# Optimization experiments

Measured on AMD Instinct MI355X. Metric: run time of the kernel, lower is better.

The kernel has to match this reference:

```python
import jax, jax.numpy as jnp
import numpy as np

EMBED_DIM = 1024
NUM_HEADS = 16
HEAD_DIM = EMBED_DIM // NUM_HEADS


def setup_inputs() -> dict:
    key = jax.random.key(0)
    ks = jax.random.split(key, 9)
    B, S, E = 2, 2048, EMBED_DIM
    lim = 1.0 / np.sqrt(E)
    def lin(kw, kb):
        W = jax.random.uniform(kw, (E, E), jnp.float32, -lim, lim)
        b = jax.random.uniform(kb, (E,), jnp.float32, -lim, lim)
        return W, b
    Wq, bq = lin(ks[0], ks[1])
    Wk, bk = lin(ks[2], ks[3])
    Wv, bv = lin(ks[4], ks[5])
    Wo, bo = lin(ks[6], ks[7])
    x = jax.random.normal(ks[8], (B, S, E), jnp.float32)
    return {"x": x, "Wq": Wq, "bq": bq, "Wk": Wk, "bk": bk,
            "Wv": Wv, "bv": bv, "Wo": Wo, "bo": bo}


def reference(x, Wq, bq, Wk, bk, Wv, bv, Wo, bo):
    B, S, E = x.shape
    H, D = NUM_HEADS, HEAD_DIM
    scale = D ** -0.5
    # projections (torch Linear: x @ W.T + b); here W stored as [in, out]-equivalent via transpose convention
    q = (x @ Wq.T + bq).reshape(B, S, H, D).transpose(0, 2, 1, 3)  # b h s d
    k = (x @ Wk.T + bk).reshape(B, S, H, D).transpose(0, 2, 1, 3)
    v = (x @ Wv.T + bv).reshape(B, S, H, D).transpose(0, 2, 1, 3)
    scores = jnp.einsum('bhqd,bhkd->bhqk', q, k) * scale
    attn = jax.nn.softmax(scores, axis=-1)
    out = jnp.einsum('bhqk,bhkd->bhqd', attn, v)
    out = out.transpose(0, 2, 1, 3).reshape(B, S, E)
    return out @ Wo.T + bo
```

## Files before the change

kernel.cpp:

```cpp
#include <hip/hip_runtime.h>


using u16 = unsigned short;
using u32 = unsigned int;

typedef __bf16 bf16x8 __attribute__((ext_vector_type(8)));
typedef float  f32x4  __attribute__((ext_vector_type(4)));
typedef float  f32x16 __attribute__((ext_vector_type(16)));
typedef u32    u32x4  __attribute__((ext_vector_type(4)));

constexpr int GB = 2;
constexpr int GS = 2048;
constexpr int GH = 16;
constexpr int GD = 64;
constexpr int GE = 1024;
constexpr int GM = GB * GS;
constexpr int PSTRIDE = 2048;

__device__ __forceinline__ u16 f2bf(float f) {
    u32 u = __float_as_uint(f);
    u += 0x7FFFu + ((u >> 16) & 1u);
    return (u16)(u >> 16);
}

__device__ __forceinline__ void plswap(u32& a, u32& b) {
#if __has_builtin(__builtin_amdgcn_permlane32_swap)
    auto r = __builtin_amdgcn_permlane32_swap(a, b, false, false);
    a = r[0]; b = r[1];
#else
    asm volatile("v_permlane32_swap_b32 %0, %1" : "+v"(a), "+v"(b));
#endif
}

__device__ __forceinline__ float xchg32(float v) {
    u32 a = __float_as_uint(v), b = a;
    plswap(a, b);
    return __uint_as_float((threadIdx.x & 32) ? a : b);
}

__device__ __forceinline__ u32 cvtpk(float lo, float hi) {
    u32 d;
    asm("v_cvt_pk_bf16_f32 %0, %1, %2" : "=v"(d) : "v"(lo), "v"(hi));
    return d;
}

__device__ __forceinline__ void gl_lds16(const u16* g, u16* l) {
#if __has_builtin(__builtin_amdgcn_global_load_lds)
    __builtin_amdgcn_global_load_lds(
        (const __attribute__((address_space(1))) void*)g,
        (__attribute__((address_space(3))) void*)l, 16, 0, 0);
#else
    *reinterpret_cast<uint4*>(l) = *reinterpret_cast<const uint4*>(g);
#endif
}

__global__ void cvt_kernel(const float* __restrict__ in, u16* __restrict__ out, int n) {
    int idx = blockIdx.x * blockDim.x + threadIdx.x;
    int stride = gridDim.x * blockDim.x;
    for (int i = idx * 4; i < n; i += stride * 4) {
        float4 f = *reinterpret_cast<const float4*>(in + i);
        ushort4 o;
        o.x = f2bf(f.x); o.y = f2bf(f.y); o.z = f2bf(f.z); o.w = f2bf(f.w);
        *reinterpret_cast<ushort4*>(out + i) = o;
    }
}

__global__ void cvtw_kernel(const float* __restrict__ w0, const float* __restrict__ w1,
                            const float* __restrict__ w2, const float* __restrict__ w3,
                            u16* __restrict__ o0, u16* __restrict__ o1,
                            u16* __restrict__ o2, u16* __restrict__ o3) {
    const float* in = blockIdx.y == 0 ? w0 : blockIdx.y == 1 ? w1 : blockIdx.y == 2 ? w2 : w3;
    u16* out = blockIdx.y == 0 ? o0 : blockIdx.y == 1 ? o1 : blockIdx.y == 2 ? o2 : o3;
    int idx = blockIdx.x * blockDim.x + threadIdx.x;
    int stride = gridDim.x * blockDim.x;
    for (int i = idx * 4; i < GE * GE; i += stride * 4) {
        float4 f = *reinterpret_cast<const float4*>(in + i);
        ushort4 o;
        o.x = f2bf(f.x); o.y = f2bf(f.y); o.z = f2bf(f.z); o.w = f2bf(f.w);
        *reinterpret_cast<ushort4*>(out + i) = o;
    }
}

__global__ __launch_bounds__(256)
void qkv_gemm(const u16* __restrict__ A,
              const u16* __restrict__ wq, const u16* __restrict__ wk, const u16* __restrict__ wv,
              const float* __restrict__ bq, const float* __restrict__ bk, const float* __restrict__ bv,
              u16* __restrict__ Qb, u16* __restrict__ Kb, u16* __restrict__ VTb) {
    constexpr int Kd = GE;
    __shared__ u16 As[128 * 32];
    __shared__ u16 Bs[128 * 32];

    const int z = blockIdx.z;
    const u16* __restrict__ Bw = z == 0 ? wq : z == 1 ? wk : wv;
    const float* __restrict__ bias = z == 0 ? bq : z == 1 ? bk : bv;
    u16* __restrict__ outp = z == 0 ? Qb : z == 1 ? Kb : VTb;

    const int tid = threadIdx.x;
    const int m0 = blockIdx.y * 128;
    const int n0 = blockIdx.x * 128;
    const int wave = tid >> 6, lane = tid & 63;
    const int wm = (wave >> 1) * 64, wn = (wave & 1) * 64;
    const int g = lane >> 4, rw = lane & 15;

    f32x4 acc[4][4] = {};

    for (int kt = 0; kt < Kd; kt += 32) {
        __syncthreads();
#pragma unroll
        for (int j = 0; j < 2; ++j) {
            int c = wave * 128 + j * 64 + lane;
            int r = c >> 2, u = (c & 3) * 8;
            gl_lds16(&A [(size_t)(m0 + r) * Kd + kt + u], &As[c * 8]);
            gl_lds16(&Bw[(size_t)(n0 + r) * Kd + kt + u], &Bs[c * 8]);
        }
        __syncthreads();

        bf16x8 aF[4], bF[4];
#pragma unroll
        for (int mf = 0; mf < 4; ++mf)
            aF[mf] = *reinterpret_cast<const bf16x8*>(&As[(wm + mf * 16 + rw) * 32 + g * 8]);
#pragma unroll
        for (int nf = 0; nf < 4; ++nf)
            bF[nf] = *reinterpret_cast<const bf16x8*>(&Bs[(wn + nf * 16 + rw) * 32 + g * 8]);
#pragma unroll
        for (int mf = 0; mf < 4; ++mf)
#pragma unroll
            for (int nf = 0; nf < 4; ++nf)
                acc[mf][nf] = __builtin_amdgcn_mfma_f32_16x16x32_bf16(aF[mf], bF[nf], acc[mf][nf], 0, 0, 0);
    }

#pragma unroll
    for (int mf = 0; mf < 4; ++mf)
#pragma unroll
        for (int nf = 0; nf < 4; ++nf)
#pragma unroll
            for (int r = 0; r < 4; ++r) {
                int m = m0 + wm + mf * 16 + g * 4 + r;
                int n = n0 + wn + nf * 16 + rw;
                u16 hv = f2bf(acc[mf][nf][r] + bias[n]);
                int b = m >> 11, s = m & (GS - 1);
                int h = n >> 6, d = n & 63;
                if (z == 2)
                    outp[(((size_t)(b * GH + h)) * GD + d) * GS + s] = hv;
                else
                    outp[(((size_t)(b * GH + h)) * GS + s) * GD + d] = hv;
            }
}

__global__ __launch_bounds__(256)
void out_gemm(const u16* __restrict__ A, const u16* __restrict__ Bw,
              const float* __restrict__ bias, float* __restrict__ outp) {
    constexpr int Kd = GE, Nd = GE;
    __shared__ u16 As[128 * 32];
    __shared__ u16 Bs[128 * 32];

    const int tid = threadIdx.x;
    const int m0 = blockIdx.y * 128;
    const int n0 = blockIdx.x * 128;
    const int wave = tid >> 6, lane = tid & 63;
    const int wm = (wave >> 1) * 64, wn = (wave & 1) * 64;
    const int g = lane >> 4, rw = lane & 15;

    f32x4 acc[4][4] = {};

    for (int kt = 0; kt < Kd; kt += 32) {
        __syncthreads();
#pragma unroll
        for (int j = 0; j < 2; ++j) {
            int c = wave * 128 + j * 64 + lane;
            int r = c >> 2, u = (c & 3) * 8;
            gl_lds16(&A [(size_t)(m0 + r) * Kd + kt + u], &As[c * 8]);
            gl_lds16(&Bw[(size_t)(n0 + r) * Kd + kt + u], &Bs[c * 8]);
        }
        __syncthreads();

        bf16x8 aF[4], bF[4];
#pragma unroll
        for (int mf = 0; mf < 4; ++mf)
            aF[mf] = *reinterpret_cast<const bf16x8*>(&As[(wm + mf * 16 + rw) * 32 + g * 8]);
#pragma unroll
        for (int nf = 0; nf < 4; ++nf)
            bF[nf] = *reinterpret_cast<const bf16x8*>(&Bs[(wn + nf * 16 + rw) * 32 + g * 8]);
#pragma unroll
        for (int mf = 0; mf < 4; ++mf)
#pragma unroll
            for (int nf = 0; nf < 4; ++nf)
                acc[mf][nf] = __builtin_amdgcn_mfma_f32_16x16x32_bf16(aF[mf], bF[nf], acc[mf][nf], 0, 0, 0);
    }

#pragma unroll
    for (int mf = 0; mf < 4; ++mf)
#pragma unroll
        for (int nf = 0; nf < 4; ++nf)
#pragma unroll
            for (int r = 0; r < 4; ++r) {
                int m = m0 + wm + mf * 16 + g * 4 + r;
                int n = n0 + wn + nf * 16 + rw;
                outp[(size_t)m * Nd + n] = acc[mf][nf][r] + bias[n];
            }
}

template <int NSPLIT>
__global__ __launch_bounds__(256)
void attn_kernel(const u16* __restrict__ Q, const u16* __restrict__ Kp,
                 const u16* __restrict__ VT, u16* __restrict__ ctx,
                 float* __restrict__ Opart, float* __restrict__ Mpart,
                 float* __restrict__ Lpart) {
    int bh, qb, split;
    if (NSPLIT == 2) {
        const int wg = (blockIdx.x & 7) * 128 + (blockIdx.x >> 3);
        bh = wg >> 5;
        split = wg & 1;
        qb = ((wg >> 1) & 15) * 128;
    } else {
        const int wg = (blockIdx.x & 7) * 64 + (blockIdx.x >> 3);
        bh = wg >> 4;
        split = 0;
        qb = (wg & 15) * 128;
    }
    const int wave = threadIdx.x >> 6;
    const int lane = threadIdx.x & 63;
    const int l31 = lane & 31;
    const int hi = lane >> 5;
    const int q0 = qb + wave * 32;
    constexpr int KVLEN = GS / NSPLIT;
    constexpr int NT2 = KVLEN / 64;
    const int kvbase = split * KVLEN;

    const u16* __restrict__ Qbh = Q  + (size_t)bh * GS * GD;
    const u16* __restrict__ Kbh = Kp + (size_t)bh * GS * GD;
    const u16* __restrict__ Vbh = VT + (size_t)bh * GD * GS;

    __shared__ u16 sK[2][4096];
    __shared__ u16 sV[2][4096];

    bf16x8 qf[4];
#pragma unroll
    for (int s = 0; s < 4; ++s)
        qf[s] = *reinterpret_cast<const bf16x8*>(
            Qbh + (size_t)(q0 + l31) * GD + hi * 8 + 16 * s);

    f32x16 O0 = {}, O1 = {};
    float m = -1e30f, lsum = 0.f;
    const float SC = 0.125f * 1.44269504088896f;

    const int c0 = wave * 128 + lane;
    const int r0 = c0 >> 3, w0 = c0 & 7;
    const int swzcol = (w0 ^ (r0 & 7)) * 8;
    const u16* kSrc = Kbh + (size_t)(kvbase + r0) * GD + swzcol;
    const u16* vSrc = Vbh + (size_t)r0 * GS + kvbase + swzcol;
    u16* const dK0 = &sK[0][c0 * 8];
    u16* const dK1 = &sK[1][c0 * 8];
    u16* const dV0 = &sV[0][c0 * 8];
    u16* const dV1 = &sV[1][c0 * 8];

    auto stageTo = [&](u16* dk, u16* dv, const u16* ks, const u16* vs) {
        gl_lds16(ks,            dk);
        gl_lds16(ks + 8 * GD,   dk + 512);
        gl_lds16(vs,            dv);
        gl_lds16(vs + 8 * GS,   dv + 512);
    };

    int offA[4];
#pragma unroll
    for (int s = 0; s < 4; ++s)
        offA[s] = l31 * 64 + (((2 * s + hi) ^ (l31 & 7)) * 8);

    auto step = [&](const u16* bK, const u16* bV) {
        f32x16 sa = {}, sb = {};
        bf16x8 ka[4], kb[4];
#pragma unroll
        for (int s = 0; s < 4; ++s) {
            ka[s] = *reinterpret_cast<const bf16x8*>(&bK[offA[s]]);
            kb[s] = *reinterpret_cast<const bf16x8*>(&bK[offA[s] + 2048]);
        }
        __builtin_amdgcn_s_setprio(1);
#pragma unroll
        for (int s = 0; s < 4; ++s) {
            sa = __builtin_amdgcn_mfma_f32_32x32x16_bf16(ka[s], qf[s], sa, 0, 0, 0);
            sb = __builtin_amdgcn_mfma_f32_32x32x16_bf16(kb[s], qf[s], sb, 0, 0, 0);
        }
        __builtin_amdgcn_s_setprio(0);

        bf16x8 vf0[4], vf1[4];
#pragma unroll
        for (int s = 0; s < 4; ++s) {
            vf0[s] = *reinterpret_cast<const bf16x8*>(&bV[offA[s]]);
            vf1[s] = *reinterpret_cast<const bf16x8*>(&bV[offA[s] + 2048]);
        }

        float t16[16];
#pragma unroll
        for (int r = 0; r < 16; ++r) t16[r] = fmaxf(sa[r], sb[r]);
        float u0 = fmaxf(fmaxf(t16[0],  t16[1]),  t16[2]);
        float u1 = fmaxf(fmaxf(t16[3],  t16[4]),  t16[5]);
        float u2 = fmaxf(fmaxf(t16[6],  t16[7]),  t16[8]);
        float u3 = fmaxf(fmaxf(t16[9],  t16[10]), t16[11]);
        float u4 = fmaxf(fmaxf(t16[12], t16[13]), t16[14]);
        float w0_ = fmaxf(fmaxf(u0, u1), u2);
        float w1_ = fmaxf(fmaxf(u3, u4), t16[15]);
        float mx = fmaxf(w0_, w1_);
        mx = fmaxf(mx, xchg32(mx));
        float mxs = mx * SC;
        if (__any(mxs > m + 8.f)) {
            float mn = fmaxf(m, mxs);
            float alpha = __builtin_amdgcn_exp2f(m - mn);
            m = mn;
            lsum *= alpha;
#pragma unroll
            for (int r = 0; r < 16; ++r) { O0[r] *= alpha; O1[r] *= alpha; }
        }
        float pa[16], pb[16];
#pragma unroll
        for (int r = 0; r < 16; ++r) {
            pa[r] = __builtin_amdgcn_exp2f(fmaf(sa[r], SC, -m));
            pb[r] = __builtin_amdgcn_exp2f(fmaf(sb[r], SC, -m));
        }
        float s16[16];
#pragma unroll
        for (int r = 0; r < 16; ++r) s16[r] = pa[r] + pb[r];
#pragma unroll
        for (int r = 0; r < 8; ++r) s16[r] += s16[r + 8];
#pragma unroll
        for (int r = 0; r < 4; ++r) s16[r] += s16[r + 4];
        lsum += (s16[0] + s16[1]) + (s16[2] + s16[3]);

        u32 wa[8], wb[8];
#pragma unroll
        for (int i = 0; i < 8; ++i) {
            wa[i] = cvtpk(pa[2 * i], pa[2 * i + 1]);
            wb[i] = cvtpk(pb[2 * i], pb[2 * i + 1]);
        }
        plswap(wa[0], wa[2]); plswap(wa[1], wa[3]);
        plswap(wa[4], wa[6]); plswap(wa[5], wa[7]);
        plswap(wb[0], wb[2]); plswap(wb[1], wb[3]);
        plswap(wb[4], wb[6]); plswap(wb[5], wb[7]);
        u32x4 a0 = {wa[0], wa[1], wa[2], wa[3]};
        u32x4 a1 = {wa[4], wa[5], wa[6], wa[7]};
        u32x4 b0 = {wb[0], wb[1], wb[2], wb[3]};
        u32x4 b1 = {wb[4], wb[5], wb[6], wb[7]};
        bf16x8 pva0 = __builtin_bit_cast(bf16x8, a0);
        bf16x8 pva1 = __builtin_bit_cast(bf16x8, a1);
        bf16x8 pvb0 = __builtin_bit_cast(bf16x8, b0);
        bf16x8 pvb1 = __builtin_bit_cast(bf16x8, b1);

        __builtin_amdgcn_s_setprio(1);
        O0 = __builtin_amdgcn_mfma_f32_32x32x16_bf16(vf0[0], pva0, O0, 0, 0, 0);
        O0 = __builtin_amdgcn_mfma_f32_32x32x16_bf16(vf0[1], pva1, O0, 0, 0, 0);
        O0 = __builtin_amdgcn_mfma_f32_32x32x16_bf16(vf0[2], pvb0, O0, 0, 0, 0);
        O0 = __builtin_amdgcn_mfma_f32_32x32x16_bf16(vf0[3], pvb1, O0, 0, 0, 0);
        O1 = __builtin_amdgcn_mfma_f32_32x32x16_bf16(vf1[0], pva0, O1, 0, 0, 0);
        O1 = __builtin_amdgcn_mfma_f32_32x32x16_bf16(vf1[1], pva1, O1, 0, 0, 0);
        O1 = __builtin_amdgcn_mfma_f32_32x32x16_bf16(vf1[2], pvb0, O1, 0, 0, 0);
        O1 = __builtin_amdgcn_mfma_f32_32x32x16_bf16(vf1[3], pvb1, O1, 0, 0, 0);
        __builtin_amdgcn_s_setprio(0);
        __syncthreads();
    };

    stageTo(dK0, dV0, kSrc, vSrc);
    kSrc += 64 * GD; vSrc += 64;
    __syncthreads();

#pragma unroll 1
    for (int t = 0; t < NT2; t += 2) {
        stageTo(dK1, dV1, kSrc, vSrc);
        kSrc += 64 * GD; vSrc += 64;
        step(sK[0], sV[0]);
        if (t + 2 < NT2) {
            stageTo(dK0, dV0, kSrc, vSrc);
            kSrc += 64 * GD; vSrc += 64;
        }
        step(sK[1], sV[1]);
    }

    lsum += xchg32(lsum);

    if (NSPLIT == 2) {
        const int wt = bh * 64 + (q0 >> 5);
        const size_t base = ((size_t)wt * 2 + split) * PSTRIDE;
#pragma unroll
        for (int r = 0; r < 16; ++r) {
            int d = (r & 3) + 8 * (r >> 2) + 4 * hi;
            Opart[base + (size_t)d * 32 + l31]        = O0[r];
            Opart[base + (size_t)(d + 32) * 32 + l31] = O1[r];
        }
        if (hi == 0) {
            Mpart[(wt * 2 + split) * 32 + l31] = m;
            Lpart[(wt * 2 + split) * 32 + l31] = lsum;
        }
    } else {
        const int bb = bh >> 4, h = bh & 15;
        const float inv = 1.0f / lsum;
        u16* crow = ctx + ((size_t)(bb * GS + q0 + l31)) * GE + h * 64;
#pragma unroll
        for (int g2 = 0; g2 < 4; ++g2) {
            ushort4 st0, st1;
            st0.x = f2bf(O0[4 * g2 + 0] * inv); st0.y = f2bf(O0[4 * g2 + 1] * inv);
            st0.z = f2bf(O0[4 * g2 + 2] * inv); st0.w = f2bf(O0[4 * g2 + 3] * inv);
            st1.x = f2bf(O1[4 * g2 + 0] * inv); st1.y = f2bf(O1[4 * g2 + 1] * inv);
            st1.z = f2bf(O1[4 * g2 + 2] * inv); st1.w = f2bf(O1[4 * g2 + 3] * inv);
            *reinterpret_cast<ushort4*>(crow + 8 * g2 + 4 * hi)      = st0;
            *reinterpret_cast<ushort4*>(crow + 32 + 8 * g2 + 4 * hi) = st1;
        }
    }
}

__global__ __launch_bounds__(256)
void combine_kernel(const float* __restrict__ Opart, const float* __restrict__ Mpart,
                    const float* __restrict__ Lpart, u16* __restrict__ ctx) {
    const int wt = blockIdx.x;
    const int bh = wt >> 6, bb = bh >> 4, h = bh & 15;
    const int q0 = (wt & 63) * 32;
    const int q = threadIdx.x & 31, db = threadIdx.x >> 5;
    const size_t b0 = (size_t)wt * 2 * PSTRIDE, b1 = b0 + PSTRIDE;

    float m0 = Mpart[(wt * 2 + 0) * 32 + q], m1 = Mpart[(wt * 2 + 1) * 32 + q];
    float l0 = Lpart[(wt * 2 + 0) * 32 + q], l1 = Lpart[(wt * 2 + 1) * 32 + q];
    float M = fmaxf(m0, m1);
    float c0 = exp2f(m0 - M), c1 = exp2f(m1 - M);
    float inv = 1.f / (c0 * l0 + c1 * l1);
    c0 *= inv; c1 *= inv;

    u16* crow = ctx + ((size_t)(bb * GS + q0 + q)) * GE + h * 64 + db * 8;
    ushort4 s0, s1;
    float o[8];
#pragma unroll
    for (int i = 0; i < 8; ++i) {
        int d = db * 8 + i;
        o[i] = c0 * Opart[b0 + (size_t)d * 32 + q] + c1 * Opart[b1 + (size_t)d * 32 + q];
    }
    s0.x = f2bf(o[0]); s0.y = f2bf(o[1]); s0.z = f2bf(o[2]); s0.w = f2bf(o[3]);
    s1.x = f2bf(o[4]); s1.y = f2bf(o[5]); s1.z = f2bf(o[6]); s1.w = f2bf(o[7]);
    *reinterpret_cast<ushort4*>(crow)     = s0;
    *reinterpret_cast<ushort4*>(crow + 4) = s1;
}

extern "C" void kernel_launch(void* const* d_in, const int* in_sizes, int n_in,
                              void* d_out, int out_size, void* d_ws, size_t ws_size,
                              hipStream_t stream) {
    (void)in_sizes; (void)n_in; (void)out_size;

    const float* x  = (const float*)d_in[0];
    const float* Wq = (const float*)d_in[1];
    const float* bq = (const float*)d_in[2];
    const float* Wk = (const float*)d_in[3];
    const float* bk = (const float*)d_in[4];
    const float* Wv = (const float*)d_in[5];
    const float* bv = (const float*)d_in[6];
    const float* Wo = (const float*)d_in[7];
    const float* bo = (const float*)d_in[8];
    float* out = (float*)d_out;

    char* ws = (char*)d_ws;
    u16* xb  = (u16*)(ws);
    u16* wqb = (u16*)(ws + (8ll  << 20));
    u16* wkb = (u16*)(ws + (10ll << 20));
    u16* wvb = (u16*)(ws + (12ll << 20));
    u16* wob = (u16*)(ws + (14ll << 20));
    u16* Qb  = (u16*)(ws + (16ll << 20));
    u16* Kb  = (u16*)(ws + (24ll << 20));
    u16* VTb = (u16*)(ws + (32ll << 20));
    u16* ctx = (u16*)(ws + (40ll << 20));
    float* Opart = (float*)(ws + (48ll << 20));
    float* Mpart = (float*)(ws + (80ll << 20));
    float* Lpart = (float*)(ws + (80ll << 20) + (512ll << 10));
    const bool split2 = ws_size >= (81ll << 20);

    cvt_kernel<<<2048, 256, 0, stream>>>(x, xb, GM * GE);
    cvtw_kernel<<<dim3(512, 4), 256, 0, stream>>>(Wq, Wk, Wv, Wo, wqb, wkb, wvb, wob);

    qkv_gemm<<<dim3(GE / 128, GM / 128, 3), 256, 0, stream>>>(
        xb, wqb, wkb, wvb, bq, bk, bv, Qb, Kb, VTb);

    if (split2) {
        attn_kernel<2><<<dim3(1024), 256, 0, stream>>>(Qb, Kb, VTb, ctx, Opart, Mpart, Lpart);
        combine_kernel<<<dim3(2048), 256, 0, stream>>>(Opart, Mpart, Lpart, ctx);
    } else {
        attn_kernel<1><<<dim3(512), 256, 0, stream>>>(Qb, Kb, VTb, ctx, Opart, Mpart, Lpart);
    }

    out_gemm<<<dim3(GE / 128, GM / 128), 256, 0, stream>>>(ctx, wob, bo, out);
}
```

Baseline: 136.0 us.

## Triple-buffer attention K/V staging and software-pipeline QK with softmax/PV

The attention loop moves from a double-buffered LDS ring to a triple-buffered one and splits each step into issueQK, readV and finish phases. The QK MFMAs for the next tile now issue before the softmax and PV work of the current tile, so matrix and vector work can overlap across tiles. Separately, the x and weight fp32-to-bf16 conversion kernels are merged into one launch. The change uses 50% more LDS per block, which may lower occupancy, and holds two sets of score and V fragments in registers at once.

New measurement: 175.6 us. 29.1% more time.

```diff
diff --git a/kernel.cpp b/kernel.cpp
--- a/kernel.cpp
+++ b/kernel.cpp
@@ -54,26 +54,19 @@
 #endif
 }
 
-__global__ void cvt_kernel(const float* __restrict__ in, u16* __restrict__ out, int n) {
+__global__ void cvt_all(const float* __restrict__ x,
+                        const float* __restrict__ w1, const float* __restrict__ w2,
+                        const float* __restrict__ w3, const float* __restrict__ w4,
+                        u16* __restrict__ ox,
+                        u16* __restrict__ o1, u16* __restrict__ o2,
+                        u16* __restrict__ o3, u16* __restrict__ o4) {
+    const int y = blockIdx.y;
+    const float* in = y == 0 ? x : y == 1 ? w1 : y == 2 ? w2 : y == 3 ? w3 : w4;
+    u16* out = y == 0 ? ox : y == 1 ? o1 : y == 2 ? o2 : y == 3 ? o3 : o4;
+    const int n = y == 0 ? GM * GE : GE * GE;
     int idx = blockIdx.x * blockDim.x + threadIdx.x;
     int stride = gridDim.x * blockDim.x;
     for (int i = idx * 4; i < n; i += stride * 4) {
-        float4 f = *reinterpret_cast<const float4*>(in + i);
-        ushort4 o;
-        o.x = f2bf(f.x); o.y = f2bf(f.y); o.z = f2bf(f.z); o.w = f2bf(f.w);
-        *reinterpret_cast<ushort4*>(out + i) = o;
-    }
-}
-
-__global__ void cvtw_kernel(const float* __restrict__ w0, const float* __restrict__ w1,
-                            const float* __restrict__ w2, const float* __restrict__ w3,
-                            u16* __restrict__ o0, u16* __restrict__ o1,
-                            u16* __restrict__ o2, u16* __restrict__ o3) {
-    const float* in = blockIdx.y == 0 ? w0 : blockIdx.y == 1 ? w1 : blockIdx.y == 2 ? w2 : w3;
-    u16* out = blockIdx.y == 0 ? o0 : blockIdx.y == 1 ? o1 : blockIdx.y == 2 ? o2 : o3;
-    int idx = blockIdx.x * blockDim.x + threadIdx.x;
-    int stride = gridDim.x * blockDim.x;
-    for (int i = idx * 4; i < GE * GE; i += stride * 4) {
         float4 f = *reinterpret_cast<const float4*>(in + i);
         ushort4 o;
         o.x = f2bf(f.x); o.y = f2bf(f.y); o.z = f2bf(f.z); o.w = f2bf(f.w);
@@ -231,8 +224,8 @@
     const u16* __restrict__ Kbh = Kp + (size_t)bh * GS * GD;
     const u16* __restrict__ Vbh = VT + (size_t)bh * GD * GS;
 
-    __shared__ u16 sK[2][4096];
-    __shared__ u16 sV[2][4096];
+    __shared__ u16 sK[3][4096];
+    __shared__ u16 sV[3][4096];
 
     bf16x8 qf[4];
 #pragma unroll
@@ -245,20 +238,17 @@
     const float SC = 0.125f * 1.44269504088896f;
 
     const int c0 = wave * 128 + lane;
-    const int r0 = c0 >> 3, w0 = c0 & 7;
-    const int swzcol = (w0 ^ (r0 & 7)) * 8;
-    const u16* kSrc = Kbh + (size_t)(kvbase + r0) * GD + swzcol;
-    const u16* vSrc = Vbh + (size_t)r0 * GS + kvbase + swzcol;
-    u16* const dK0 = &sK[0][c0 * 8];
-    u16* const dK1 = &sK[1][c0 * 8];
-    u16* const dV0 = &sV[0][c0 * 8];
-    u16* const dV1 = &sV[1][c0 * 8];
-
-    auto stageTo = [&](u16* dk, u16* dv, const u16* ks, const u16* vs) {
-        gl_lds16(ks,            dk);
-        gl_lds16(ks + 8 * GD,   dk + 512);
-        gl_lds16(vs,            dv);
-        gl_lds16(vs + 8 * GS,   dv + 512);
+    const int r0 = c0 >> 3, w0c = c0 & 7;
+    const int swzcol = (w0c ^ (r0 & 7)) * 8;
+    const u16* kStage = Kbh + (size_t)(kvbase + r0) * GD + swzcol;
+    const u16* vStage = Vbh + (size_t)r0 * GS + kvbase + swzcol;
+
+    auto stageTo = [&](int b) {
+        gl_lds16(kStage,          &sK[b][c0 * 8]);
+        gl_lds16(kStage + 8 * GD, &sK[b][c0 * 8 + 512]);
+        gl_lds16(vStage,          &sV[b][c0 * 8]);
+        gl_lds16(vStage + 8 * GS, &sV[b][c0 * 8 + 512]);
+        kStage += 64 * GD; vStage += 64;
     };
 
     int offA[4];
@@ -266,14 +256,14 @@
     for (int s = 0; s < 4; ++s)
         offA[s] = l31 * 64 + (((2 * s + hi) ^ (l31 & 7)) * 8);
 
-    auto step = [&](const u16* bK, const u16* bV) {
-        f32x16 sa = {}, sb = {};
+    auto issueQK = [&](int b, f32x16& sa, f32x16& sb) {
         bf16x8 ka[4], kb[4];
 #pragma unroll
         for (int s = 0; s < 4; ++s) {
-            ka[s] = *reinterpret_cast<const bf16x8*>(&bK[offA[s]]);
-            kb[s] = *reinterpret_cast<const bf16x8*>(&bK[offA[s] + 2048]);
-        }
+            ka[s] = *reinterpret_cast<const bf16x8*>(&sK[b][offA[s]]);
+            kb[s] = *reinterpret_cast<const bf16x8*>(&sK[b][offA[s] + 2048]);
+        }
+        sa = f32x16{}; sb = f32x16{};
         __builtin_amdgcn_s_setprio(1);
 #pragma unroll
         for (int s = 0; s < 4; ++s) {
@@ -281,14 +271,18 @@
             sb = __builtin_amdgcn_mfma_f32_32x32x16_bf16(kb[s], qf[s], sb, 0, 0, 0);
         }
         __builtin_amdgcn_s_setprio(0);
-
-        bf16x8 vf0[4], vf1[4];
+    };
+
+    auto readV = [&](int b, bf16x8* vf0, bf16x8* vf1) {
 #pragma unroll
         for (int s = 0; s < 4; ++s) {
-            vf0[s] = *reinterpret_cast<const bf16x8*>(&bV[offA[s]]);
-            vf1[s] = *reinterpret_cast<const bf16x8*>(&bV[offA[s] + 2048]);
-        }
-
+            vf0[s] = *reinterpret_cast<const bf16x8*>(&sV[b][offA[s]]);
+            vf1[s] = *reinterpret_cast<const bf16x8*>(&sV[b][offA[s] + 2048]);
+        }
+    };
+
+    auto finish = [&](const f32x16& sa, const f32x16& sb,
+                      const bf16x8* vf0, const bf16x8* vf1) {
         float t16[16];
 #pragma unroll
         for (int r = 0; r < 16; ++r) t16[r] = fmaxf(sa[r], sb[r]);
@@ -354,23 +348,29 @@
         O1 = __builtin_amdgcn_mfma_f32_32x32x16_bf16(vf1[2], pvb0, O1, 0, 0, 0);
         O1 = __builtin_amdgcn_mfma_f32_32x32x16_bf16(vf1[3], pvb1, O1, 0, 0, 0);
         __builtin_amdgcn_s_setprio(0);
-        __syncthreads();
     };
 
-    stageTo(dK0, dV0, kSrc, vSrc);
-    kSrc += 64 * GD; vSrc += 64;
+    f32x16 saA, sbA, saB, sbB;
+    bf16x8 vA0[4], vA1[4], vB0[4], vB1[4];
+
+    stageTo(0);
+    stageTo(1);
     __syncthreads();
+    issueQK(0, saA, sbA);
+    readV(0, vA0, vA1);
 
 #pragma unroll 1
     for (int t = 0; t < NT2; t += 2) {
-        stageTo(dK1, dV1, kSrc, vSrc);
-        kSrc += 64 * GD; vSrc += 64;
-        step(sK[0], sV[0]);
-        if (t + 2 < NT2) {
-            stageTo(dK0, dV0, kSrc, vSrc);
-            kSrc += 64 * GD; vSrc += 64;
-        }
-        step(sK[1], sV[1]);
+        if (t + 2 < NT2) stageTo((t + 2) % 3);
+        if (t + 1 < NT2) issueQK((t + 1) % 3, saB, sbB);
+        finish(saA, sbA, vA0, vA1);
+        if (t + 1 < NT2) readV((t + 1) % 3, vB0, vB1);
+        __syncthreads();
+        if (t + 3 < NT2) stageTo((t + 3) % 3);
+        if (t + 2 < NT2) issueQK((t + 2) % 3, saA, sbA);
+        if (t + 1 < NT2) finish(saB, sbB, vB0, vB1);
+        if (t + 2 < NT2) readV((t + 2) % 3, vA0, vA1);
+        __syncthreads();
     }
 
     lsum += xchg32(lsum);
@@ -466,8 +466,8 @@
     float* Lpart = (float*)(ws + (80ll << 20) + (512ll << 10));
     const bool split2 = ws_size >= (81ll << 20);
 
-    cvt_kernel<<<2048, 256, 0, stream>>>(x, xb, GM * GE);
-    cvtw_kernel<<<dim3(512, 4), 256, 0, stream>>>(Wq, Wk, Wv, Wo, wqb, wkb, wvb, wob);
+    cvt_all<<<dim3(1024, 5), 256, 0, stream>>>(x, Wq, Wk, Wv, Wo,
+                                               xb, wqb, wkb, wvb, wob);
 
     qkv_gemm<<<dim3(GE / 128, GM / 128, 3), 256, 0, stream>>>(
         xb, wqb, wkb, wvb, bq, bk, bv, Qb, Kb, VTb);
```

## Merge conversion kernels and use BK=64 XOR-swizzled LDS tiles in GEMMs

Applied to the files above, without the earlier changes.

Combines the x and weight fp32-to-bf16 conversions into one launch with a 5-row grid, removing one kernel launch. Both projection GEMMs double the K tile to 64, which halves the number of barrier pairs per K loop. They also XOR-swizzle the LDS column placement so fragment reads avoid bank conflicts. LDS use per block grows from 16KB to 32KB, which may reduce occupancy, and the load path remains single-buffered.

After: 151.5 us. 1.11x slower.

```diff
diff --git a/kernel.cpp b/kernel.cpp
--- a/kernel.cpp
+++ b/kernel.cpp
@@ -54,7 +54,16 @@
 #endif
 }
 
-__global__ void cvt_kernel(const float* __restrict__ in, u16* __restrict__ out, int n) {
+__global__ void cvt_all(const float* __restrict__ x,
+                        const float* __restrict__ w1, const float* __restrict__ w2,
+                        const float* __restrict__ w3, const float* __restrict__ w4,
+                        u16* __restrict__ ox,
+                        u16* __restrict__ o1, u16* __restrict__ o2,
+                        u16* __restrict__ o3, u16* __restrict__ o4) {
+    const int y = blockIdx.y;
+    const float* in = y == 0 ? x : y == 1 ? w1 : y == 2 ? w2 : y == 3 ? w3 : w4;
+    u16* out = y == 0 ? ox : y == 1 ? o1 : y == 2 ? o2 : y == 3 ? o3 : o4;
+    const int n = y == 0 ? GM * GE : GE * GE;
     int idx = blockIdx.x * blockDim.x + threadIdx.x;
     int stride = gridDim.x * blockDim.x;
     for (int i = idx * 4; i < n; i += stride * 4) {
@@ -65,30 +74,14 @@
     }
 }
 
-__global__ void cvtw_kernel(const float* __restrict__ w0, const float* __restrict__ w1,
-                            const float* __restrict__ w2, const float* __restrict__ w3,
-                            u16* __restrict__ o0, u16* __restrict__ o1,
-                            u16* __restrict__ o2, u16* __restrict__ o3) {
-    const float* in = blockIdx.y == 0 ? w0 : blockIdx.y == 1 ? w1 : blockIdx.y == 2 ? w2 : w3;
-    u16* out = blockIdx.y == 0 ? o0 : blockIdx.y == 1 ? o1 : blockIdx.y == 2 ? o2 : o3;
-    int idx = blockIdx.x * blockDim.x + threadIdx.x;
-    int stride = gridDim.x * blockDim.x;
-    for (int i = idx * 4; i < GE * GE; i += stride * 4) {
-        float4 f = *reinterpret_cast<const float4*>(in + i);
-        ushort4 o;
-        o.x = f2bf(f.x); o.y = f2bf(f.y); o.z = f2bf(f.z); o.w = f2bf(f.w);
-        *reinterpret_cast<ushort4*>(out + i) = o;
-    }
-}
-
 __global__ __launch_bounds__(256)
 void qkv_gemm(const u16* __restrict__ A,
               const u16* __restrict__ wq, const u16* __restrict__ wk, const u16* __restrict__ wv,
               const float* __restrict__ bq, const float* __restrict__ bk, const float* __restrict__ bv,
               u16* __restrict__ Qb, u16* __restrict__ Kb, u16* __restrict__ VTb) {
-    constexpr int Kd = GE;
-    __shared__ u16 As[128 * 32];
-    __shared__ u16 Bs[128 * 32];
+    constexpr int Kd = GE, BK = 64;
+    __shared__ u16 As[128 * BK];
+    __shared__ u16 Bs[128 * BK];
 
     const int z = blockIdx.z;
     const u16* __restrict__ Bw = z == 0 ? wq : z == 1 ? wk : wv;
@@ -104,29 +97,39 @@
 
     f32x4 acc[4][4] = {};
 
-    for (int kt = 0; kt < Kd; kt += 32) {
+    for (int kt = 0; kt < Kd; kt += BK) {
         __syncthreads();
 #pragma unroll
-        for (int j = 0; j < 2; ++j) {
-            int c = wave * 128 + j * 64 + lane;
-            int r = c >> 2, u = (c & 3) * 8;
-            gl_lds16(&A [(size_t)(m0 + r) * Kd + kt + u], &As[c * 8]);
-            gl_lds16(&Bw[(size_t)(n0 + r) * Kd + kt + u], &Bs[c * 8]);
+        for (int j = 0; j < 4; ++j) {
+            int c = j * 256 + tid;
+            int r = c >> 3, w = c & 7;
+            int sc = (w ^ (r & 7)) * 8;
+            gl_lds16(&A [(size_t)(m0 + r) * Kd + kt + sc], &As[c * 8]);
+            gl_lds16(&Bw[(size_t)(n0 + r) * Kd + kt + sc], &Bs[c * 8]);
         }
         __syncthreads();
 
-        bf16x8 aF[4], bF[4];
-#pragma unroll
-        for (int mf = 0; mf < 4; ++mf)
-            aF[mf] = *reinterpret_cast<const bf16x8*>(&As[(wm + mf * 16 + rw) * 32 + g * 8]);
-#pragma unroll
-        for (int nf = 0; nf < 4; ++nf)
-            bF[nf] = *reinterpret_cast<const bf16x8*>(&Bs[(wn + nf * 16 + rw) * 32 + g * 8]);
-#pragma unroll
-        for (int mf = 0; mf < 4; ++mf)
-#pragma unroll
-            for (int nf = 0; nf < 4; ++nf)
-                acc[mf][nf] = __builtin_amdgcn_mfma_f32_16x16x32_bf16(aF[mf], bF[nf], acc[mf][nf], 0, 0, 0);
+#pragma unroll
+        for (int kk = 0; kk < 2; ++kk) {
+            bf16x8 aF[4], bF[4];
+#pragma unroll
+            for (int mf = 0; mf < 4; ++mf) {
+                int row = wm + mf * 16 + rw;
+                aF[mf] = *reinterpret_cast<const bf16x8*>(
+                    &As[row * BK + (((kk * 4 + g) ^ (row & 7)) * 8)]);
+            }
+#pragma unroll
+            for (int nf = 0; nf < 4; ++nf) {
+                int row = wn + nf * 16 + rw;
+                bF[nf] = *reinterpret_cast<const bf16x8*>(
+                    &Bs[row * BK + (((kk * 4 + g) ^ (row & 7)) * 8)]);
+            }
+#pragma unroll
+            for (int mf = 0; mf < 4; ++mf)
+#pragma unroll
+                for (int nf = 0; nf < 4; ++nf)
+                    acc[mf][nf] = __builtin_amdgcn_mfma_f32_16x16x32_bf16(aF[mf], bF[nf], acc[mf][nf], 0, 0, 0);
+        }
     }
 
 #pragma unroll
@@ -150,9 +153,9 @@
 __global__ __launch_bounds__(256)
 void out_gemm(const u16* __restrict__ A, const u16* __restrict__ Bw,
               const float* __restrict__ bias, float* __restrict__ outp) {
-    constexpr int Kd = GE, Nd = GE;
-    __shared__ u16 As[128 * 32];
-    __shared__ u16 Bs[128 * 32];
+    constexpr int Kd = GE, Nd = GE, BK = 64;
+    __shared__ u16 As[128 * BK];
+    __shared__ u16 Bs[128 * BK];
 
     const int tid = threadIdx.x;
     const int m0 = blockIdx.y * 128;
@@ -163,29 +166,39 @@
 
     f32x4 acc[4][4] = {};
 
-    for (int kt = 0; kt < Kd; kt += 32) {
+    for (int kt = 0; kt < Kd; kt += BK) {
         __syncthreads();
 #pragma unroll
-        for (int j = 0; j < 2; ++j) {
-            int c = wave * 128 + j * 64 + lane;
-            int r = c >> 2, u = (c & 3) * 8;
-            gl_lds16(&A [(size_t)(m0 + r) * Kd + kt + u], &As[c * 8]);
-            gl_lds16(&Bw[(size_t)(n0 + r) * Kd + kt + u], &Bs[c * 8]);
+        for (int j = 0; j < 4; ++j) {
+            int c = j * 256 + tid;
+            int r = c >> 3, w = c & 7;
+            int sc = (w ^ (r & 7)) * 8;
+            gl_lds16(&A [(size_t)(m0 + r) * Kd + kt + sc], &As[c * 8]);
+            gl_lds16(&Bw[(size_t)(n0 + r) * Kd + kt + sc], &Bs[c * 8]);
         }
         __syncthreads();
 
-        bf16x8 aF[4], bF[4];
-#pragma unroll
-        for (int mf = 0; mf < 4; ++mf)
-            aF[mf] = *reinterpret_cast<const bf16x8*>(&As[(wm + mf * 16 + rw) * 32 + g * 8]);
-#pragma unroll
-        for (int nf = 0; nf < 4; ++nf)
-            bF[nf] = *reinterpret_cast<const bf16x8*>(&Bs[(wn + nf * 16 + rw) * 32 + g * 8]);
-#pragma unroll
-        for (int mf = 0; mf < 4; ++mf)
-#pragma unroll
-            for (int nf = 0; nf < 4; ++nf)
-                acc[mf][nf] = __builtin_amdgcn_mfma_f32_16x16x32_bf16(aF[mf], bF[nf], acc[mf][nf], 0, 0, 0);
+#pragma unroll
+        for (int kk = 0; kk < 2; ++kk) {
+            bf16x8 aF[4], bF[4];
+#pragma unroll
+            for (int mf = 0; mf < 4; ++mf) {
+                int row = wm + mf * 16 + rw;
+                aF[mf] = *reinterpret_cast<const bf16x8*>(
+                    &As[row * BK + (((kk * 4 + g) ^ (row & 7)) * 8)]);
+            }
+#pragma unroll
+            for (int nf = 0; nf < 4; ++nf) {
+                int row = wn + nf * 16 + rw;
+                bF[nf] = *reinterpret_cast<const bf16x8*>(
+                    &Bs[row * BK + (((kk * 4 + g) ^ (row & 7)) * 8)]);
+            }
+#pragma unroll
+            for (int mf = 0; mf < 4; ++mf)
+#pragma unroll
+                for (int nf = 0; nf < 4; ++nf)
+                    acc[mf][nf] = __builtin_amdgcn_mfma_f32_16x16x32_bf16(aF[mf], bF[nf], acc[mf][nf], 0, 0, 0);
+        }
     }
 
 #pragma unroll
@@ -245,8 +258,8 @@
     const float SC = 0.125f * 1.44269504088896f;
 
     const int c0 = wave * 128 + lane;
-    const int r0 = c0 >> 3, w0 = c0 & 7;
-    const int swzcol = (w0 ^ (r0 & 7)) * 8;
+    const int r0 = c0 >> 3, w0c = c0 & 7;
+    const int swzcol = (w0c ^ (r0 & 7)) * 8;
     const u16* kSrc = Kbh + (size_t)(kvbase + r0) * GD + swzcol;
     const u16* vSrc = Vbh + (size_t)r0 * GS + kvbase + swzcol;
     u16* const dK0 = &sK[0][c0 * 8];
@@ -466,8 +479,8 @@
     float* Lpart = (float*)(ws + (80ll << 20) + (512ll << 10));
     const bool split2 = ws_size >= (81ll << 20);
 
-    cvt_kernel<<<2048, 256, 0, stream>>>(x, xb, GM * GE);
-    cvtw_kernel<<<dim3(512, 4), 256, 0, stream>>>(Wq, Wk, Wv, Wo, wqb, wkb, wvb, wob);
+    cvt_all<<<dim3(1024, 5), 256, 0, stream>>>(x, Wq, Wk, Wv, Wo,
+                                               xb, wqb, wkb, wvb, wob);
 
     qkv_gemm<<<dim3(GE / 128, GM / 128, 3), 256, 0, stream>>>(
         xb, wqb, wkb, wvb, bq, bk, bv, Qb, Kb, VTb);
```
